# Performance work log

Measured on AMD Instinct MI355X. Metric: run time of the kernel, lower is better.

The kernel has to match this reference:

```python
import jax, jax.numpy as jnp
import numpy as np

N_NODES = 100000
N_EDGES = 800000
NFEAT, NHID, NCLASS = 500, 64, 16


def _spmm(src, dst, edge_w, feat, n_nodes):
    # sparse adj @ feat:  out[i] = sum_{e: dst[e]=i} edge_w[e] * feat[src[e]]
    gathered = edge_w[:, None] * feat[src]  # [E, F]
    return jax.ops.segment_sum(gathered, dst, num_segments=n_nodes)


def setup_inputs() -> dict:
    key = jax.random.key(0)
    ks = jax.random.split(key, 8)
    return {
        "x": jax.random.normal(ks[0], (N_NODES, NFEAT), dtype=jnp.float32),
        "W1": jax.random.normal(ks[1], (NFEAT, NHID), dtype=jnp.float32) / np.sqrt(NFEAT),
        "b1": jax.random.normal(ks[2], (NHID,), dtype=jnp.float32) * 0.01,
        "W2": jax.random.normal(ks[3], (NHID, NCLASS), dtype=jnp.float32) / np.sqrt(NHID),
        "b2": jax.random.normal(ks[4], (NCLASS,), dtype=jnp.float32) * 0.01,
        "edge_w": jax.random.uniform(ks[5], (N_EDGES,), dtype=jnp.float32),
        "src": jax.random.randint(ks[6], (N_EDGES,), 0, N_NODES, dtype=jnp.int32),
        "dst": jax.random.randint(ks[7], (N_EDGES,), 0, N_NODES, dtype=jnp.int32),
    }


def reference(x, W1, b1, W2, b2, edge_w, src, dst):
    n = x.shape[0]
    # Layer 1: GraphConvolution -> ReLU (dropout is identity in eval mode)
    h = jax.nn.relu(_spmm(src, dst, edge_w, x @ W1, n) + b1)
    # Layer 2: GraphConvolution
    out = _spmm(src, dst, edge_w, h @ W2, n) + b2
    return out
```

## Files before the change

kernel.cpp:

```cpp
#include <hip/hip_runtime.h>

#define NN 100000
#define NE 800000
#define NF 500
#define NH 64
#define NC 16
#define SCAN_B 98
#define G1TILES 782
#define ROLEB 224

typedef __attribute__((ext_vector_type(4))) float f32x4;
typedef __attribute__((ext_vector_type(8))) short bf16x8;

__device__ __forceinline__ unsigned int f2bf(float f) {
    union { float f; unsigned int u; } v; v.f = f;
    return (v.u + 0x7FFFu + ((v.u >> 16) & 1u)) >> 16;
}
__device__ __forceinline__ unsigned int pkbf(float a, float b) {
    return f2bf(a) | (f2bf(b) << 16);
}
__device__ __forceinline__ float bfbits_lo(unsigned int u) { return __uint_as_float(u << 16); }
__device__ __forceinline__ float bfbits_hi(unsigned int u) { return __uint_as_float(u & 0xffff0000u); }

#define GLOAD_LDS16(g, l) __builtin_amdgcn_global_load_lds(                      \
    (const __attribute__((address_space(1))) void*)(g),                          \
    (__attribute__((address_space(3))) void*)(l), 16, 0, 0)

__device__ __forceinline__ void acc_fp8x8(float* a, const uint2 v, const float w) {
    a[0] += w * __builtin_amdgcn_cvt_f32_fp8(v.x, 0);
    a[1] += w * __builtin_amdgcn_cvt_f32_fp8(v.x, 1);
    a[2] += w * __builtin_amdgcn_cvt_f32_fp8(v.x, 2);
    a[3] += w * __builtin_amdgcn_cvt_f32_fp8(v.x, 3);
    a[4] += w * __builtin_amdgcn_cvt_f32_fp8(v.y, 0);
    a[5] += w * __builtin_amdgcn_cvt_f32_fp8(v.y, 1);
    a[6] += w * __builtin_amdgcn_cvt_f32_fp8(v.y, 2);
    a[7] += w * __builtin_amdgcn_cvt_f32_fp8(v.y, 3);
}

__global__ __launch_bounds__(256) void k_zero(int4* __restrict__ p) {
    int i = blockIdx.x * 256 + threadIdx.x;
    if (i < NN / 4) p[i] = make_int4(0, 0, 0, 0);
}

__global__ __launch_bounds__(1024) void k_scanA(const int* __restrict__ deg, int* __restrict__ bsum) {
    __shared__ int s[1024];
    int t = threadIdx.x, i = blockIdx.x * 1024 + t;
    s[t] = (i < NN) ? deg[i] : 0;
    __syncthreads();
    for (int off = 512; off > 0; off >>= 1) {
        if (t < off) s[t] += s[t + off];
        __syncthreads();
    }
    if (t == 0) bsum[blockIdx.x] = s[0];
}

__global__ __launch_bounds__(1024) void k_scanC(const int* __restrict__ deg, const int* __restrict__ bsum,
                                                int* __restrict__ start, int* __restrict__ cursor) {
    __shared__ int s[1024];
    __shared__ int bs[128];
    int t = threadIdx.x, i = blockIdx.x * 1024 + t;
    if (t < 128) bs[t] = (t < SCAN_B) ? bsum[t] : 0;
    int d = (i < NN) ? deg[i] : 0;
    s[t] = d;
    __syncthreads();
    for (int off = 1; off < 128; off <<= 1) {
        int u = 0;
        if (t < 128 && t >= off) u = bs[t - off];
        __syncthreads();
        if (t < 128 && t >= off) bs[t] += u;
        __syncthreads();
    }
    for (int off = 1; off < 1024; off <<= 1) {
        int u = (t >= off) ? s[t - off] : 0;
        __syncthreads();
        s[t] += u;
        __syncthreads();
    }
    int base = (blockIdx.x == 0) ? 0 : bs[blockIdx.x - 1];
    if (i < NN) {
        int ex = base + s[t] - d;
        start[i] = ex;
        cursor[i] = ex;
    }
    if (blockIdx.x == SCAN_B - 1 && t == 0) start[NN] = bs[SCAN_B - 1];
}

__global__ void k_scatter(const int* __restrict__ src, const int* __restrict__ dst,
                          const float* __restrict__ ew, int* __restrict__ cursor,
                          int2* __restrict__ edges) {
    int e = blockIdx.x * 256 + threadIdx.x;
    if (e < NE) {
        int p = atomicAdd(&cursor[dst[e]], 1);
        edges[p] = make_int2(src[e], __float_as_int(ew[e]));
    }
}

__global__ __launch_bounds__(256) void k_g1(const float* __restrict__ x,
                                            const float* __restrict__ W1,
                                            unsigned char* __restrict__ h1f,
                                            const int* __restrict__ dst, int* __restrict__ deg) {
    __shared__ float xs[128 * 64];
    __shared__ unsigned short ws[64 * 64];
    const int bid = blockIdx.x, tid = threadIdx.x;
    if (bid >= G1TILES) {
        int rb = bid - G1TILES;
        for (int e = rb * 256 + tid; e < NE; e += ROLEB * 256)
            atomicAdd(&deg[dst[e]], 1);
        return;
    }
    const int lane = tid & 63;
    const int wv   = tid >> 6;
    const int row0 = bid * 128;

    f32x4 acc[2][4];
#pragma unroll
    for (int i = 0; i < 2; ++i)
#pragma unroll
        for (int j = 0; j < 4; ++j) acc[i][j] = (f32x4){0.f, 0.f, 0.f, 0.f};

    const int lr    = lane >> 4;
    const int lsl   = (lane & 15) >> 1;
    const int lhalf = lane & 1;
    const long maxidx = (long)NN * NF - 4;

    for (int kt = 0; kt < 8; ++kt) {
        const int k0 = kt * 64;
#pragma unroll
        for (int i = 0; i < 8; ++i) {
            int r  = wv * 32 + i * 4 + lr;
            int gm = row0 + r; if (gm >= NN) gm = NN - 1;
            long gi = (long)gm * NF + k0 + ((lsl ^ (r & 7)) << 3) + (lhalf << 2);
            if (gi > maxidx) gi = maxidx;
            GLOAD_LDS16(x + gi, xs + (wv * 32 + i * 4) * 64);
        }
#pragma unroll
        for (int p = 0; p < 2; ++p) {
            int u  = tid + p * 256;
            int n  = u & 63, sl = u >> 6;
            int gk = k0 + sl * 8;
            float e[8];
#pragma unroll
            for (int j = 0; j < 8; ++j)
                e[j] = (gk + j < NF) ? W1[(long)(gk + j) * NH + n] : 0.f;
            uint4 pk;
            pk.x = pkbf(e[0], e[1]);
            pk.y = pkbf(e[2], e[3]);
            pk.z = pkbf(e[4], e[5]);
            pk.w = pkbf(e[6], e[7]);
            *(uint4*)(ws + n * 64 + (sl ^ (n & 7)) * 8) = pk;
        }
        __syncthreads();
#pragma unroll
        for (int ks = 0; ks < 2; ++ks) {
            const int kg = ks * 4 + (lane >> 4);
            bf16x8 af[2], bfr[4];
#pragma unroll
            for (int i = 0; i < 2; ++i) {
                int r = wv * 32 + i * 16 + (lane & 15);
                const float* srcp = xs + r * 64 + ((kg ^ (r & 7)) << 3);
                f32x4 lo = *(const f32x4*)(srcp);
                f32x4 hi = *(const f32x4*)(srcp + 4);
                uint4 pk;
                pk.x = pkbf(lo[0], lo[1]);
                pk.y = pkbf(lo[2], lo[3]);
                pk.z = pkbf(hi[0], hi[1]);
                pk.w = pkbf(hi[2], hi[3]);
                af[i] = *(bf16x8*)&pk;
            }
#pragma unroll
            for (int j = 0; j < 4; ++j) {
                int n = j * 16 + (lane & 15);
                bfr[j] = *(const bf16x8*)(ws + n * 64 + (kg ^ (n & 7)) * 8);
            }
#pragma unroll
            for (int i = 0; i < 2; ++i)
#pragma unroll
                for (int j = 0; j < 4; ++j)
                    acc[i][j] = __builtin_amdgcn_mfma_f32_16x16x32_bf16(af[i], bfr[j], acc[i][j], 0, 0, 0);
        }
        __syncthreads();
    }
    unsigned char* xb = (unsigned char*)xs;
    const int c = lane & 15;
#pragma unroll
    for (int i = 0; i < 2; ++i) {
#pragma unroll
        for (int q = 0; q < 4; ++q) {
            int r = wv * 32 + i * 16 + (lane >> 4) * 4 + q;
            int pk01 = __builtin_amdgcn_cvt_pk_fp8_f32(acc[i][0][q], acc[i][1][q], 0, false);
            int pk23 = __builtin_amdgcn_cvt_pk_fp8_f32(acc[i][2][q], acc[i][3][q], 0, false);
            xb[r * 64 + 0 * 16 + c] = (unsigned char)(pk01 & 0xff);
            xb[r * 64 + 1 * 16 + c] = (unsigned char)((pk01 >> 8) & 0xff);
            xb[r * 64 + 2 * 16 + c] = (unsigned char)(pk23 & 0xff);
            xb[r * 64 + 3 * 16 + c] = (unsigned char)((pk23 >> 8) & 0xff);
        }
    }
    __syncthreads();
    {
        int rr = tid >> 1, off = (tid & 1) * 32;
        int gm = row0 + rr;
        if (gm < NN) {
            uint4 a = *(uint4*)(xb + rr * 64 + off);
            uint4 b = *(uint4*)(xb + rr * 64 + off + 16);
            *(uint4*)(h1f + (long)gm * 64 + off)      = a;
            *(uint4*)(h1f + (long)gm * 64 + off + 16) = b;
        }
    }
}

__global__ __launch_bounds__(256) void k_l1(const int* __restrict__ start,
                                            const int2* __restrict__ edges,
                                            const unsigned char* __restrict__ h1f,
                                            const float* __restrict__ b1,
                                            const float* __restrict__ W2,
                                            unsigned short* __restrict__ h2b) {
    __shared__ float w2s[NH * NC];
    const int tid = threadIdx.x;
    const float4 w2stage = *(const float4*)(W2 + tid * 4);

    const int lane = tid & 63;
    const int wid  = ((blockIdx.x * 256 + tid) >> 6) * 2 + (lane >> 5);
    const int fo   = lane & 7;
    const int es   = (lane >> 3) & 3;

    const int s = start[wid], e = start[wid + 1];
    float a[8] = {0.f, 0.f, 0.f, 0.f, 0.f, 0.f, 0.f, 0.f};
    int p = s + es;
    while (p < e) {
        const int i1 = p + 4, i2 = p + 8, i3 = p + 12;
        const bool b1 = i1 < e, b2 = i2 < e, b3 = i3 < e;
        const int2 r0 = edges[p];
        const int2 r1 = edges[b1 ? i1 : p];
        const int2 r2 = edges[b2 ? i2 : p];
        const int2 r3 = edges[b3 ? i3 : p];
        const uint2 v0 = *(const uint2*)(h1f + (long)r0.x * 64 + fo * 8);
        const uint2 v1 = *(const uint2*)(h1f + (long)r1.x * 64 + fo * 8);
        const uint2 v2 = *(const uint2*)(h1f + (long)r2.x * 64 + fo * 8);
        const uint2 v3 = *(const uint2*)(h1f + (long)r3.x * 64 + fo * 8);
        acc_fp8x8(a, v0, __int_as_float(r0.y));
        acc_fp8x8(a, v1, b1 ? __int_as_float(r1.y) : 0.f);
        acc_fp8x8(a, v2, b2 ? __int_as_float(r2.y) : 0.f);
        acc_fp8x8(a, v3, b3 ? __int_as_float(r3.y) : 0.f);
        p += 16;
    }
    *(float4*)(w2s + tid * 4) = w2stage;
    __syncthreads();
#pragma unroll
    for (int m = 8; m <= 16; m <<= 1)
#pragma unroll
        for (int j = 0; j < 8; ++j) a[j] += __shfl_xor(a[j], m, 64);
    const float4 ba = *(const float4*)(b1 + fo * 8);
    const float4 bb = *(const float4*)(b1 + fo * 8 + 4);
    float r[8];
    r[0] = fmaxf(a[0] + ba.x, 0.f); r[1] = fmaxf(a[1] + ba.y, 0.f);
    r[2] = fmaxf(a[2] + ba.z, 0.f); r[3] = fmaxf(a[3] + ba.w, 0.f);
    r[4] = fmaxf(a[4] + bb.x, 0.f); r[5] = fmaxf(a[5] + bb.y, 0.f);
    r[6] = fmaxf(a[6] + bb.z, 0.f); r[7] = fmaxf(a[7] + bb.w, 0.f);
    float p0 = 0.f, p1 = 0.f, p2 = 0.f, p3 = 0.f;
#pragma unroll
    for (int j = 0; j < 8; ++j) {
        const f32x4 wv = *(const f32x4*)(w2s + (fo * 8 + j) * NC + es * 4);
        p0 += r[j] * wv[0]; p1 += r[j] * wv[1];
        p2 += r[j] * wv[2]; p3 += r[j] * wv[3];
    }
#pragma unroll
    for (int m = 1; m <= 4; m <<= 1) {
        p0 += __shfl_xor(p0, m, 64); p1 += __shfl_xor(p1, m, 64);
        p2 += __shfl_xor(p2, m, 64); p3 += __shfl_xor(p3, m, 64);
    }
    if (fo == 0) {
        uint2 pk;
        pk.x = pkbf(p0, p1);
        pk.y = pkbf(p2, p3);
        *(uint2*)(h2b + (long)wid * NC + es * 4) = pk;
    }
}

__global__ __launch_bounds__(256) void k_spmm2(const int* __restrict__ start,
                                               const int2* __restrict__ edges,
                                               const unsigned short* __restrict__ h2b,
                                               const float* __restrict__ b2,
                                               float* __restrict__ out) {
    const int lane = threadIdx.x & 63;
    const int wid  = ((blockIdx.x * 256 + threadIdx.x) >> 6) * 4 + (lane >> 4);
    const int es   = (lane >> 2) & 3;
    const int f4   = lane & 3;
    const int s = start[wid], e = start[wid + 1];
    float4 acc = make_float4(0.f, 0.f, 0.f, 0.f);
    int p = s + es;
    while (p < e) {
        const int i1 = p + 4, i2 = p + 8, i3 = p + 12;
        const bool b1 = i1 < e, b2 = i2 < e, b3 = i3 < e;
        const int2 r0 = edges[p];
        const int2 r1 = edges[b1 ? i1 : p];
        const int2 r2 = edges[b2 ? i2 : p];
        const int2 r3 = edges[b3 ? i3 : p];
        const uint2 v0 = *(const uint2*)(h2b + (long)r0.x * NC + f4 * 4);
        const uint2 v1 = *(const uint2*)(h2b + (long)r1.x * NC + f4 * 4);
        const uint2 v2 = *(const uint2*)(h2b + (long)r2.x * NC + f4 * 4);
        const uint2 v3 = *(const uint2*)(h2b + (long)r3.x * NC + f4 * 4);
        const float w0 = __int_as_float(r0.y);
        const float w1 = b1 ? __int_as_float(r1.y) : 0.f;
        const float w2 = b2 ? __int_as_float(r2.y) : 0.f;
        const float w3 = b3 ? __int_as_float(r3.y) : 0.f;
        acc.x += w0 * bfbits_lo(v0.x); acc.y += w0 * bfbits_hi(v0.x);
        acc.z += w0 * bfbits_lo(v0.y); acc.w += w0 * bfbits_hi(v0.y);
        acc.x += w1 * bfbits_lo(v1.x); acc.y += w1 * bfbits_hi(v1.x);
        acc.z += w1 * bfbits_lo(v1.y); acc.w += w1 * bfbits_hi(v1.y);
        acc.x += w2 * bfbits_lo(v2.x); acc.y += w2 * bfbits_hi(v2.x);
        acc.z += w2 * bfbits_lo(v2.y); acc.w += w2 * bfbits_hi(v2.y);
        acc.x += w3 * bfbits_lo(v3.x); acc.y += w3 * bfbits_hi(v3.x);
        acc.z += w3 * bfbits_lo(v3.y); acc.w += w3 * bfbits_hi(v3.y);
        p += 16;
    }
#pragma unroll
    for (int m = 4; m <= 8; m <<= 1) {
        acc.x += __shfl_xor(acc.x, m, 64); acc.y += __shfl_xor(acc.y, m, 64);
        acc.z += __shfl_xor(acc.z, m, 64); acc.w += __shfl_xor(acc.w, m, 64);
    }
    if (es == 0) {
        const float4 b = *(const float4*)(b2 + f4 * 4);
        float4 r;
        r.x = acc.x + b.x; r.y = acc.y + b.y;
        r.z = acc.z + b.z; r.w = acc.w + b.w;
        *(float4*)(out + (long)wid * NC + f4 * 4) = r;
    }
}

extern "C" void kernel_launch(void* const* d_in, const int* in_sizes, int n_in,
                              void* d_out, int out_size, void* d_ws, size_t ws_size,
                              hipStream_t stream) {
    const float* x   = (const float*)d_in[0];
    const float* W1  = (const float*)d_in[1];
    const float* b1  = (const float*)d_in[2];
    const float* W2  = (const float*)d_in[3];
    const float* b2  = (const float*)d_in[4];
    const float* ew  = (const float*)d_in[5];
    const int*   src = (const int*)d_in[6];
    const int*   dst = (const int*)d_in[7];
    float* out = (float*)d_out;

    char* w = (char*)d_ws;
    unsigned char*  h1f = (unsigned char*)(w + 0);
    unsigned short* h2b = (unsigned short*)(w + 25600000);
    int*   bsum   = (int*) (w + 32000000);
    int*   startp = (int*) (w + 32001024);
    int*   cursor = (int*) (w + 32402048);
    int2*  edges  = (int2*)(w + 32803072);

    k_zero   <<<(NN / 4 + 255) / 256, 256, 0, stream>>>((int4*)cursor);
    k_g1     <<<G1TILES + ROLEB, 256, 0, stream>>>(x, W1, h1f, dst, cursor);
    k_scanA  <<<SCAN_B, 1024, 0, stream>>>(cursor, bsum);
    k_scanC  <<<SCAN_B, 1024, 0, stream>>>(cursor, bsum, startp, cursor);
    k_scatter<<<(NE + 255) / 256, 256, 0, stream>>>(src, dst, ew, cursor, edges);
    k_l1     <<<(NN / 2 * 64) / 256, 256, 0, stream>>>(startp, edges, h1f, b1, W2, h2b);
    k_spmm2  <<<(NN / 4 * 64) / 256, 256, 0, stream>>>(startp, edges, h2b, b2, out);
}
```

Measured before the change: 156.3 us.

## Move edge scatter into GEMM kernel and run degree histogram beforehand

The degree histogram becomes a standalone kernel that runs before the scan. The CSR scatter (atomic cursor increment plus edge write) now runs on the extra blocks of the layer-1 GEMM kernel, overlapping with the dense x@W1 work instead of the histogram. This removes the separate scatter kernel launch but adds a histogram launch, leaving the launch count unchanged. The intent is to hide the scatter's atomic and random-write cost behind the GEMM's bandwidth-bound work rather than the cheaper histogram.

```diff
diff --git a/kernel.cpp b/kernel.cpp
--- a/kernel.cpp
+++ b/kernel.cpp
@@ -40,6 +40,11 @@
 __global__ __launch_bounds__(256) void k_zero(int4* __restrict__ p) {
     int i = blockIdx.x * 256 + threadIdx.x;
     if (i < NN / 4) p[i] = make_int4(0, 0, 0, 0);
+}
+
+__global__ void k_hist(const int* __restrict__ dst, int* __restrict__ deg) {
+    int e = blockIdx.x * 256 + threadIdx.x;
+    if (e < NE) atomicAdd(&deg[dst[e]], 1);
 }
 
 __global__ __launch_bounds__(1024) void k_scanA(const int* __restrict__ deg, int* __restrict__ bsum) {
@@ -85,27 +90,21 @@
     if (blockIdx.x == SCAN_B - 1 && t == 0) start[NN] = bs[SCAN_B - 1];
 }
 
-__global__ void k_scatter(const int* __restrict__ src, const int* __restrict__ dst,
-                          const float* __restrict__ ew, int* __restrict__ cursor,
-                          int2* __restrict__ edges) {
-    int e = blockIdx.x * 256 + threadIdx.x;
-    if (e < NE) {
-        int p = atomicAdd(&cursor[dst[e]], 1);
-        edges[p] = make_int2(src[e], __float_as_int(ew[e]));
-    }
-}
-
 __global__ __launch_bounds__(256) void k_g1(const float* __restrict__ x,
                                             const float* __restrict__ W1,
                                             unsigned char* __restrict__ h1f,
-                                            const int* __restrict__ dst, int* __restrict__ deg) {
+                                            const int* __restrict__ src, const int* __restrict__ dst,
+                                            const float* __restrict__ ew,
+                                            int* __restrict__ cursor, int2* __restrict__ edges) {
     __shared__ float xs[128 * 64];
     __shared__ unsigned short ws[64 * 64];
     const int bid = blockIdx.x, tid = threadIdx.x;
     if (bid >= G1TILES) {
         int rb = bid - G1TILES;
-        for (int e = rb * 256 + tid; e < NE; e += ROLEB * 256)
-            atomicAdd(&deg[dst[e]], 1);
+        for (int e = rb * 256 + tid; e < NE; e += ROLEB * 256) {
+            int p = atomicAdd(&cursor[dst[e]], 1);
+            edges[p] = make_int2(src[e], __float_as_int(ew[e]));
+        }
         return;
     }
     const int lane = tid & 63;
@@ -228,19 +227,19 @@
     int p = s + es;
     while (p < e) {
         const int i1 = p + 4, i2 = p + 8, i3 = p + 12;
-        const bool b1 = i1 < e, b2 = i2 < e, b3 = i3 < e;
+        const bool b1c = i1 < e, b2c = i2 < e, b3c = i3 < e;
         const int2 r0 = edges[p];
-        const int2 r1 = edges[b1 ? i1 : p];
-        const int2 r2 = edges[b2 ? i2 : p];
-        const int2 r3 = edges[b3 ? i3 : p];
+        const int2 r1 = edges[b1c ? i1 : p];
+        const int2 r2 = edges[b2c ? i2 : p];
+        const int2 r3 = edges[b3c ? i3 : p];
         const uint2 v0 = *(const uint2*)(h1f + (long)r0.x * 64 + fo * 8);
         const uint2 v1 = *(const uint2*)(h1f + (long)r1.x * 64 + fo * 8);
         const uint2 v2 = *(const uint2*)(h1f + (long)r2.x * 64 + fo * 8);
         const uint2 v3 = *(const uint2*)(h1f + (long)r3.x * 64 + fo * 8);
         acc_fp8x8(a, v0, __int_as_float(r0.y));
-        acc_fp8x8(a, v1, b1 ? __int_as_float(r1.y) : 0.f);
-        acc_fp8x8(a, v2, b2 ? __int_as_float(r2.y) : 0.f);
-        acc_fp8x8(a, v3, b3 ? __int_as_float(r3.y) : 0.f);
+        acc_fp8x8(a, v1, b1c ? __int_as_float(r1.y) : 0.f);
+        acc_fp8x8(a, v2, b2c ? __int_as_float(r2.y) : 0.f);
+        acc_fp8x8(a, v3, b3c ? __int_as_float(r3.y) : 0.f);
         p += 16;
     }
     *(float4*)(w2s + tid * 4) = w2stage;
@@ -290,19 +289,19 @@
     int p = s + es;
     while (p < e) {
         const int i1 = p + 4, i2 = p + 8, i3 = p + 12;
-        const bool b1 = i1 < e, b2 = i2 < e, b3 = i3 < e;
+        const bool b1c = i1 < e, b2c = i2 < e, b3c = i3 < e;
         const int2 r0 = edges[p];
-        const int2 r1 = edges[b1 ? i1 : p];
-        const int2 r2 = edges[b2 ? i2 : p];
-        const int2 r3 = edges[b3 ? i3 : p];
+        const int2 r1 = edges[b1c ? i1 : p];
+        const int2 r2 = edges[b2c ? i2 : p];
+        const int2 r3 = edges[b3c ? i3 : p];
         const uint2 v0 = *(const uint2*)(h2b + (long)r0.x * NC + f4 * 4);
         const uint2 v1 = *(const uint2*)(h2b + (long)r1.x * NC + f4 * 4);
         const uint2 v2 = *(const uint2*)(h2b + (long)r2.x * NC + f4 * 4);
         const uint2 v3 = *(const uint2*)(h2b + (long)r3.x * NC + f4 * 4);
         const float w0 = __int_as_float(r0.y);
-        const float w1 = b1 ? __int_as_float(r1.y) : 0.f;
-        const float w2 = b2 ? __int_as_float(r2.y) : 0.f;
-        const float w3 = b3 ? __int_as_float(r3.y) : 0.f;
+        const float w1 = b1c ? __int_as_float(r1.y) : 0.f;
+        const float w2 = b2c ? __int_as_float(r2.y) : 0.f;
+        const float w3 = b3c ? __int_as_float(r3.y) : 0.f;
         acc.x += w0 * bfbits_lo(v0.x); acc.y += w0 * bfbits_hi(v0.x);
         acc.z += w0 * bfbits_lo(v0.y); acc.w += w0 * bfbits_hi(v0.y);
         acc.x += w1 * bfbits_lo(v1.x); acc.y += w1 * bfbits_hi(v1.x);
@@ -348,11 +347,11 @@
     int*   cursor = (int*) (w + 32402048);
     int2*  edges  = (int2*)(w + 32803072);
 
-    k_zero   <<<(NN / 4 + 255) / 256, 256, 0, stream>>>((int4*)cursor);
-    k_g1     <<<G1TILES + ROLEB, 256, 0, stream>>>(x, W1, h1f, dst, cursor);
-    k_scanA  <<<SCAN_B, 1024, 0, stream>>>(cursor, bsum);
-    k_scanC  <<<SCAN_B, 1024, 0, stream>>>(cursor, bsum, startp, cursor);
-    k_scatter<<<(NE + 255) / 256, 256, 0, stream>>>(src, dst, ew, cursor, edges);
-    k_l1     <<<(NN / 2 * 64) / 256, 256, 0, stream>>>(startp, edges, h1f, b1, W2, h2b);
-    k_spmm2  <<<(NN / 4 * 64) / 256, 256, 0, stream>>>(startp, edges, h2b, b2, out);
-}
+    k_zero  <<<(NN / 4 + 255) / 256, 256, 0, stream>>>((int4*)cursor);
+    k_hist  <<<(NE + 255) / 256, 256, 0, stream>>>(dst, cursor);
+    k_scanA <<<SCAN_B, 1024, 0, stream>>>(cursor, bsum);
+    k_scanC <<<SCAN_B, 1024, 0, stream>>>(cursor, bsum, startp, cursor);
+    k_g1    <<<G1TILES + ROLEB, 256, 0, stream>>>(x, W1, h1f, src, dst, ew, cursor, edges);
+    k_l1    <<<(NN / 2 * 64) / 256, 256, 0, stream>>>(startp, edges, h1f, b1, W2, h2b);
+    k_spmm2 <<<(NN / 4 * 64) / 256, 256, 0, stream>>>(startp, edges, h2b, b2, out);
+}
```

After: 153.4 us. About the same (-1.9%).
